# Kernel tuning notes

Measured on AMD Instinct MI355X. Metric: run time of the kernel, lower is better.

## Reference

```python
import jax, jax.numpy as jnp
import numpy as np

N = 32768          # nodes
LEVELS = 4         # num_sign_hops + 1
NUM_FEATURES = 512
HIDDEN = 512
VQ_DIM = 64
CODEBOOK_SIZE = 4096
VQ_WEIGHT = 0.25   # commitment_weight


def setup_inputs() -> dict:
    key = jax.random.key(0)
    ks = jax.random.split(key, 11)
    s = 0.02
    return {
        "x": jax.random.normal(ks[0], (N, LEVELS, NUM_FEATURES), jnp.float32),
        # per-level encoder: Linear(F,512) -> ReLU -> Linear(512,D)
        "enc_w1": jax.random.normal(ks[1], (LEVELS, NUM_FEATURES, HIDDEN), jnp.float32) * s,
        "enc_b1": jnp.zeros((LEVELS, HIDDEN), jnp.float32),
        "enc_w2": jax.random.normal(ks[2], (LEVELS, HIDDEN, VQ_DIM), jnp.float32) * s,
        "enc_b2": jnp.zeros((LEVELS, VQ_DIM), jnp.float32),
        # per-level decoder: Linear(D,512) -> ReLU -> Linear(512,F)
        "dec_w1": jax.random.normal(ks[3], (LEVELS, VQ_DIM, HIDDEN), jnp.float32) * s,
        "dec_b1": jnp.zeros((LEVELS, HIDDEN), jnp.float32),
        "dec_w2": jax.random.normal(ks[4], (LEVELS, HIDDEN, NUM_FEATURES), jnp.float32) * s,
        "dec_b2": jnp.zeros((LEVELS, NUM_FEATURES), jnp.float32),
        # per-level EMA codebooks (constants w.r.t. gradient in the torch module)
        "codebook": jax.random.normal(ks[5], (LEVELS, CODEBOOK_SIZE, VQ_DIM), jnp.float32),
    }


def reference(x, enc_w1, enc_b1, enc_w2, enc_b2,
              dec_w1, dec_b1, dec_w2, dec_b2, codebook):
    # Faithful to Quantizer.forward (eval mode: dropout = identity; EMA codebook
    # update is a training-time side effect, not part of the returned math).
    L = x.shape[1]
    total_mse = jnp.float32(0.0)
    commit_last = jnp.float32(0.0)
    for l in range(L):  # small fixed level count, structurally distinct params
        xl = x[:, l, :]                                   # [N, F]
        h = jax.nn.relu(xl @ enc_w1[l] + enc_b1[l])       # [N, 512]
        z = h @ enc_w2[l] + enc_b2[l]                     # [N, D]
        cb = codebook[l]                                  # [K, D]
        # squared euclidean distances [N, K] (cdist^2 via expansion)
        d = ((z * z).sum(-1, keepdims=True)
             - 2.0 * (z @ cb.T)
             + (cb * cb).sum(-1)[None, :])
        idx = jnp.argmin(d, axis=-1)                      # [N]
        q = cb[idx]                                       # [N, D] codebook lookup
        # commitment loss: mse(stop_grad(quantize), z) * weight
        commit = VQ_WEIGHT * jnp.mean((jax.lax.stop_gradient(q) - z) ** 2)
        # straight-through estimator
        quant = z + jax.lax.stop_gradient(q - z)
        h2 = jax.nn.relu(quant @ dec_w1[l] + dec_b1[l])   # [N, 512]
        x_hat = h2 @ dec_w2[l] + dec_b2[l]                # [N, F]
        total_mse = total_mse + jnp.mean((x_hat - xl) ** 2)
        commit_last = commit  # original returns LAST level's commit_loss / levels
    return (total_mse / L, commit_last / L)
```

## Files before the change

kernel.cpp:

```cpp
#include <hip/hip_runtime.h>

#define NS 32768
#define NLEV 4
#define NF 512
#define HID 512
#define VQD 64
#define CBS 4096

typedef __attribute__((ext_vector_type(8))) short bf16x8;
typedef __attribute__((ext_vector_type(4))) float f32x4;

__device__ inline unsigned short f2bf(float f) {
    unsigned int u = __float_as_uint(f);
    unsigned int r = (u + 0x7FFFu + ((u >> 16) & 1u)) >> 16;
    return (unsigned short)r;
}

__device__ __forceinline__ void gl16(const void* g, void* l) {
    __builtin_amdgcn_global_load_lds(
        (const __attribute__((address_space(1))) unsigned int*)g,
        (__attribute__((address_space(3))) unsigned int*)l, 16, 0, 0);
}


__global__ void transpose_all(const float* __restrict__ ew1, const float* __restrict__ ew2,
                              const float* __restrict__ dw1, const float* __restrict__ dw2,
                              unsigned short* __restrict__ ew1t, unsigned short* __restrict__ ew2t,
                              unsigned short* __restrict__ dw1t, unsigned short* __restrict__ dw2t) {
    long i = (long)blockIdx.x * 256 + threadIdx.x;
    const long s1 = (long)NLEV * NF * HID;
    const long s2 = (long)NLEV * HID * VQD;
    const long s3 = (long)NLEV * VQD * HID;
    const long s4 = (long)NLEV * HID * NF;
    const float* src;
    unsigned short* dst;
    int R, C;
    if (i < s1) { src = ew1; dst = ew1t; R = NF; C = HID; }
    else if (i < s1 + s2) { i -= s1; src = ew2; dst = ew2t; R = HID; C = VQD; }
    else if (i < s1 + s2 + s3) { i -= s1 + s2; src = dw1; dst = dw1t; R = VQD; C = HID; }
    else if (i < s1 + s2 + s3 + s4) { i -= s1 + s2 + s3; src = dw2; dst = dw2t; R = HID; C = NF; }
    else return;
    int r = (int)(i % R);
    long t = i / R;
    int c = (int)(t % C);
    int b = (int)(t / C);
    dst[i] = f2bf(src[((long)b * R + r) * C + c]);
}

__global__ void cb_prep(const float* __restrict__ cb, unsigned short* __restrict__ cbb,
                        float* __restrict__ cbn) {
    int i = blockIdx.x * 256 + threadIdx.x;
    if (i >= NLEV * CBS) return;
    const float* row = cb + (long)i * VQD;
    float s = 0.f;
    for (int k = 0; k < VQD; k++) {
        float v = row[k];
        s += v * v;
        cbb[(long)i * VQD + k] = f2bf(v);
    }
    cbn[i] = s;
}

__global__ void xconv(const float* __restrict__ x, unsigned short* __restrict__ xb) {
    long i = (long)blockIdx.x * 256 + threadIdx.x;
    int l = (int)(i / ((long)NS * (NF / 8)));
    long rem = i % ((long)NS * (NF / 8));
    int n = (int)(rem >> 6);
    int f8 = ((int)rem & 63) * 8;
    const float* src = x + ((long)n * NLEV + l) * NF + f8;
    float4 f0 = *(const float4*)src;
    float4 f1 = *(const float4*)(src + 4);
    short t[8];
    t[0] = (short)f2bf(f0.x); t[1] = (short)f2bf(f0.y); t[2] = (short)f2bf(f0.z); t[3] = (short)f2bf(f0.w);
    t[4] = (short)f2bf(f1.x); t[5] = (short)f2bf(f1.y); t[6] = (short)f2bf(f1.z); t[7] = (short)f2bf(f1.w);
    *(int4*)(xb + ((long)l * NS + n) * NF + f8) = *(const int4*)t;
}

template <int NT, int NTOT, int RELU, int OUT_MODE, int GATHER>
__global__ __launch_bounds__(256) void gemm128(
    const unsigned short* __restrict__ Ab, long astride, long abatch,
    const int* __restrict__ idx,
    const unsigned short* __restrict__ Bt, long bbatch,
    const float* __restrict__ bias, long biasbatch,
    unsigned short* __restrict__ Cb, float* __restrict__ Cf, long cbatch,
    const float* __restrict__ Xref, long xstride, long xbatch,
    float* __restrict__ accum, int K) {
    constexpr int BN = NT * 32;
    constexpr int NBPAN = NTOT / BN;
    constexpr int BNP = BN + 8;
    constexpr int SMEM = (128 * 32 + BN * 32) > (64 * BNP) ? (128 * 32 + BN * 32) : (64 * BNP);
    __shared__ __align__(16) short smem[SMEM];
    short* As = smem;
    short* Bs = smem + 128 * 32;
    __shared__ float red[4];

    const int bid = blockIdx.x;
    const int mblk = bid & 255;
    const int panel = bid >> 8;
    const int n_blk = panel % NBPAN;
    const int lvl = panel / NBPAN;

    Ab += (long)lvl * abatch;
    Bt += (long)lvl * bbatch;
    bias += (long)lvl * biasbatch;
    if (OUT_MODE == 0 || OUT_MODE == 1) Cb += (long)lvl * cbatch;
    if (OUT_MODE == 1) Cf += (long)lvl * cbatch;
    if (OUT_MODE == 2) Xref += (long)lvl * xbatch;
    if (GATHER) idx += (long)lvl * NS;

    const int tid = threadIdx.x;
    const int m0 = mblk * 128;
    const int n0 = n_blk * BN;
    const int wave = tid >> 6, lane = tid & 63, quad = lane >> 4, lr = lane & 15;
    const int wm = wave >> 1, wn = wave & 1;
    const int lrow = lane >> 2;
    const int lcol = (lane & 3) * 8;

    f32x4 acc[4][NT];
#pragma unroll
    for (int i = 0; i < 4; i++)
#pragma unroll
        for (int j = 0; j < NT; j++) acc[i][j] = (f32x4){0.f, 0.f, 0.f, 0.f};

    for (int k0 = 0; k0 < K; k0 += 32) {
        if (GATHER) {
            int r0 = m0 + wave * 16 + lrow;
            gl16(Ab + (long)idx[r0] * K + k0 + lcol, &As[(wave * 16) * 32]);
            gl16(Ab + (long)idx[r0 + 64] * K + k0 + lcol, &As[(64 + wave * 16) * 32]);
        } else {
            const unsigned short* ga = Ab + (long)(m0 + wave * 16 + lrow) * astride + k0 + lcol;
            gl16(ga, &As[(wave * 16) * 32]);
            gl16(ga + 64 * astride, &As[(64 + wave * 16) * 32]);
        }
        const unsigned short* gb = Bt + (long)(n0 + wave * 16 + lrow) * K + k0 + lcol;
        gl16(gb, &Bs[(wave * 16) * 32]);
        if (NT == 4) gl16(gb + 64 * (long)K, &Bs[(64 + wave * 16) * 32]);
        __syncthreads();

        bf16x8 af[4], bfr[NT];
#pragma unroll
        for (int mt = 0; mt < 4; mt++)
            af[mt] = *(const bf16x8*)&As[(wm * 64 + mt * 16 + lr) * 32 + quad * 8];
#pragma unroll
        for (int nt = 0; nt < NT; nt++)
            bfr[nt] = *(const bf16x8*)&Bs[(wn * NT * 16 + nt * 16 + lr) * 32 + quad * 8];
#pragma unroll
        for (int mt = 0; mt < 4; mt++)
#pragma unroll
            for (int nt = 0; nt < NT; nt++)
                acc[mt][nt] = __builtin_amdgcn_mfma_f32_16x16x32_bf16(af[mt], bfr[nt], acc[mt][nt], 0, 0, 0);
        __syncthreads();
    }

    float bvs[NT];
#pragma unroll
    for (int nt = 0; nt < NT; nt++) bvs[nt] = bias[n0 + wn * NT * 16 + nt * 16 + lr];

    if (OUT_MODE == 2) {
        float lsum = 0.f;
#pragma unroll
        for (int nt = 0; nt < NT; nt++) {
            int col = n0 + wn * NT * 16 + nt * 16 + lr;
#pragma unroll
            for (int mt = 0; mt < 4; mt++) {
#pragma unroll
                for (int r = 0; r < 4; r++) {
                    int row = m0 + wm * 64 + mt * 16 + quad * 4 + r;
                    float v = acc[mt][nt][r] + bvs[nt];
                    float d = v - Xref[(long)row * xstride + col];
                    lsum += d * d;
                }
            }
        }
#pragma unroll
        for (int off = 32; off; off >>= 1) lsum += __shfl_down(lsum, off, 64);
        if (lane == 0) red[wave] = lsum;
        __syncthreads();
        if (tid == 0) atomicAdd(accum, red[0] + red[1] + red[2] + red[3]);
    } else {
        short* Ct = smem;
#pragma unroll
        for (int p = 0; p < 2; p++) {
            __syncthreads();
            if (wm == p) {
#pragma unroll
                for (int nt = 0; nt < NT; nt++) {
                    int cl = wn * NT * 16 + nt * 16 + lr;
#pragma unroll
                    for (int mt = 0; mt < 4; mt++) {
#pragma unroll
                        for (int r = 0; r < 4; r++) {
                            int rl = mt * 16 + quad * 4 + r;
                            float v = acc[mt][nt][r] + bvs[nt];
                            if (RELU) v = v > 0.f ? v : 0.f;
                            Ct[rl * BNP + cl] = (short)f2bf(v);
                        }
                    }
                }
            }
            __syncthreads();
            constexpr int PER = (64 * BN / 8) / 256;
#pragma unroll
            for (int j = 0; j < PER; j++) {
                int id = j * 256 + tid;
                int row = id / (BN / 8);
                int seg = id % (BN / 8);
                int4 raw;
                short tmp[8];
                *(int4*)tmp = *(const int4*)&Ct[row * BNP + seg * 8];
                raw = *(const int4*)tmp;
                int rg = m0 + p * 64 + row;
                int cg = n0 + seg * 8;
                *(int4*)&Cb[(long)rg * NTOT + cg] = raw;
                if (OUT_MODE == 1) {
                    float f[8];
#pragma unroll
                    for (int e = 0; e < 8; e++)
                        f[e] = __uint_as_float(((unsigned int)(unsigned short)tmp[e]) << 16);
                    *(float4*)&Cf[(long)rg * NTOT + cg] = (float4){f[0], f[1], f[2], f[3]};
                    *(float4*)&Cf[(long)rg * NTOT + cg + 4] = (float4){f[4], f[5], f[6], f[7]};
                }
            }
        }
    }
}

__global__ __launch_bounds__(256) void vq_argmin(const unsigned short* __restrict__ Zb,
                                                 const unsigned short* __restrict__ cbb,
                                                 const float* __restrict__ cbn,
                                                 int* __restrict__ idxo) {
    __shared__ __align__(16) short Zs[2 * 128 * 32];
    __shared__ __align__(16) short Cs[2 * 64 * 32];
    const int lvl = blockIdx.y;
    Zb += (long)lvl * NS * VQD;
    cbb += (long)lvl * CBS * VQD;
    cbn += (long)lvl * CBS;
    idxo += (long)lvl * NS;
    const int tid = threadIdx.x;
    const int m0 = blockIdx.x * 128;
    const int wave = tid >> 6, lane = tid & 63, quad = lane >> 4, lr = lane & 15;
    const int lrow = lane >> 2, lcol = (lane & 3) * 8;

#pragma unroll
    for (int j = 0; j < 4; j++) {
        int f = tid * 4 + j;
        int p = f >> 9;
        int rem = f & 511;
        int r = rem >> 2;
        int c = (rem & 3) * 8;
        ((int4*)Zs)[f] = *(const int4*)(Zb + (long)(m0 + r) * VQD + p * 32 + c);
    }
    __syncthreads();
    bf16x8 a[2][2];
#pragma unroll
    for (int h = 0; h < 2; h++)
#pragma unroll
        for (int p = 0; p < 2; p++)
            a[h][p] = *(const bf16x8*)&Zs[p * 4096 + (h * 64 + wave * 16 + lr) * 32 + quad * 8];

    float minv[2][4] = {{1e30f, 1e30f, 1e30f, 1e30f}, {1e30f, 1e30f, 1e30f, 1e30f}};
    int mini[2][4] = {{0, 0, 0, 0}, {0, 0, 0, 0}};

    for (int nb = 0; nb < CBS; nb += 64) {
        __syncthreads();
#pragma unroll
        for (int i = 0; i < 2; i++) {
            int s = i * 4 + wave;
            int p = s >> 2;
            int r0 = (s & 3) * 16;
            gl16(cbb + (long)(nb + r0 + lrow) * VQD + p * 32 + lcol, &Cs[s * 512]);
        }
        __syncthreads();
#pragma unroll
        for (int nt = 0; nt < 4; nt++) {
            bf16x8 b0 = *(const bf16x8*)&Cs[(nt * 16 + lr) * 32 + quad * 8];
            bf16x8 b1 = *(const bf16x8*)&Cs[2048 + (nt * 16 + lr) * 32 + quad * 8];
            int n = nb + nt * 16 + lr;
            float cn = cbn[n];
#pragma unroll
            for (int h = 0; h < 2; h++) {
                f32x4 acc = {0.f, 0.f, 0.f, 0.f};
                acc = __builtin_amdgcn_mfma_f32_16x16x32_bf16(a[h][0], b0, acc, 0, 0, 0);
                acc = __builtin_amdgcn_mfma_f32_16x16x32_bf16(a[h][1], b1, acc, 0, 0, 0);
#pragma unroll
                for (int r = 0; r < 4; r++) {
                    float d = cn - 2.0f * acc[r];
                    if (d < minv[h][r]) {
                        minv[h][r] = d;
                        mini[h][r] = n;
                    }
                }
            }
        }
    }
#pragma unroll
    for (int h = 0; h < 2; h++)
#pragma unroll
        for (int r = 0; r < 4; r++) {
            float v = minv[h][r];
            int ix = mini[h][r];
#pragma unroll
            for (int off = 8; off; off >>= 1) {
                float ov = __shfl_xor(v, off, 64);
                int oi = __shfl_xor(ix, off, 64);
                if (ov < v || (ov == v && oi < ix)) {
                    v = ov;
                    ix = oi;
                }
            }
            if (lr == 0) idxo[m0 + h * 64 + wave * 16 + quad * 4 + r] = ix;
        }
}

__global__ __launch_bounds__(256) void commit_k(const int* __restrict__ idx,
                                                const float* __restrict__ cbf,
                                                const float* __restrict__ zf,
                                                float* __restrict__ accum) {
    int m = blockIdx.x * 256 + threadIdx.x;
    int id = idx[m];
    const float* c = cbf + (long)id * VQD;
    const float* z = zf + (long)m * VQD;
    float s = 0.f;
#pragma unroll
    for (int k = 0; k < VQD; k++) {
        float d = c[k] - z[k];
        s += d * d;
    }
    int lane = threadIdx.x & 63;
#pragma unroll
    for (int off = 32; off; off >>= 1) s += __shfl_down(s, off, 64);
    if (lane == 0) atomicAdd(accum, s);
}

__global__ void finalize_k(const float* __restrict__ accum, float* __restrict__ out) {
    out[0] = accum[0] / ((float)NS * NF * NLEV);
    out[1] = 0.25f * accum[1] / ((float)NS * VQD * NLEV);
}

extern "C" void kernel_launch(void* const* d_in, const int* in_sizes, int n_in, void* d_out,
                              int out_size, void* d_ws, size_t ws_size, hipStream_t stream) {
    const float* x = (const float*)d_in[0];
    const float* enc_w1 = (const float*)d_in[1];
    const float* enc_b1 = (const float*)d_in[2];
    const float* enc_w2 = (const float*)d_in[3];
    const float* enc_b2 = (const float*)d_in[4];
    const float* dec_w1 = (const float*)d_in[5];
    const float* dec_b1 = (const float*)d_in[6];
    const float* dec_w2 = (const float*)d_in[7];
    const float* dec_b2 = (const float*)d_in[8];
    const float* cb = (const float*)d_in[9];

    char* ws = (char*)d_ws;
    size_t o = 0;
    float* accum = (float*)(ws + o); o += 256;
    unsigned short* enc_w1t = (unsigned short*)(ws + o); o += (size_t)NLEV * HID * NF * 2;
    unsigned short* enc_w2t = (unsigned short*)(ws + o); o += (size_t)NLEV * VQD * HID * 2;
    unsigned short* dec_w1t = (unsigned short*)(ws + o); o += (size_t)NLEV * HID * VQD * 2;
    unsigned short* dec_w2t = (unsigned short*)(ws + o); o += (size_t)NLEV * NF * HID * 2;
    unsigned short* cbb = (unsigned short*)(ws + o); o += (size_t)NLEV * CBS * VQD * 2;
    float* cbn = (float*)(ws + o); o += (size_t)NLEV * CBS * 4;
    unsigned short* xb = (unsigned short*)(ws + o); o += (size_t)NLEV * NS * NF * 2;
    unsigned short* hb = (unsigned short*)(ws + o); o += (size_t)NLEV * NS * HID * 2;
    float* zf = (float*)(ws + o); o += (size_t)NLEV * NS * VQD * 4;
    unsigned short* zb = (unsigned short*)(ws + o); o += (size_t)NLEV * NS * VQD * 2;
    int* idxp = (int*)(ws + o); o += (size_t)NLEV * NS * 4;
    unsigned short* h2b = xb;

    hipMemsetAsync(accum, 0, 8, stream);

    transpose_all<<<(2 * NLEV * NF * HID + 2 * NLEV * HID * VQD + 255) / 256, 256, 0, stream>>>(
        enc_w1, enc_w2, dec_w1, dec_w2, enc_w1t, enc_w2t, dec_w1t, dec_w2t);
    cb_prep<<<(NLEV * CBS + 255) / 256, 256, 0, stream>>>(cb, cbb, cbn);
    xconv<<<(int)(((long)NLEV * NS * (NF / 8) + 255) / 256), 256, 0, stream>>>(x, xb);

    const int gBig = 256 * (HID / 128) * NLEV;
    const int gZ = 256 * 1 * NLEV;
    dim3 gVQ(NS / 128, NLEV);

    gemm128<4, HID, 1, 0, 0><<<gBig, 256, 0, stream>>>(
        xb, NF, (long)NS * NF, nullptr,
        enc_w1t, (long)HID * NF, enc_b1, HID,
        hb, nullptr, (long)NS * HID, nullptr, 0, 0, nullptr, NF);
    gemm128<2, VQD, 0, 1, 0><<<gZ, 256, 0, stream>>>(
        hb, HID, (long)NS * HID, nullptr,
        enc_w2t, (long)VQD * HID, enc_b2, VQD,
        zb, zf, (long)NS * VQD, nullptr, 0, 0, nullptr, HID);
    vq_argmin<<<gVQ, 256, 0, stream>>>(zb, cbb, cbn, idxp);
    commit_k<<<NS / 256, 256, 0, stream>>>(idxp + (long)(NLEV - 1) * NS,
                                           cb + (long)(NLEV - 1) * CBS * VQD,
                                           zf + (long)(NLEV - 1) * NS * VQD, accum + 1);
    gemm128<4, HID, 1, 0, 1><<<gBig, 256, 0, stream>>>(
        cbb, 0, (long)CBS * VQD, idxp,
        dec_w1t, (long)HID * VQD, dec_b1, HID,
        h2b, nullptr, (long)NS * HID, nullptr, 0, 0, nullptr, VQD);
    gemm128<4, NF, 0, 2, 0><<<gBig, 256, 0, stream>>>(
        h2b, HID, (long)NS * HID, nullptr,
        dec_w2t, (long)NF * HID, dec_b2, NF,
        nullptr, nullptr, 0, x, (long)NLEV * NF, NF, accum, HID);

    finalize_k<<<1, 1, 0, stream>>>(accum, (float*)d_out);
}
```

Measured before the change: 934.1 us.

## Fuse encoder output GEMM with VQ argmin and commit loss; deepen GEMM k-stage

```diff
diff --git a/kernel.cpp b/kernel.cpp
--- a/kernel.cpp
+++ b/kernel.cpp
@@ -14,6 +14,9 @@
     unsigned int u = __float_as_uint(f);
     unsigned int r = (u + 0x7FFFu + ((u >> 16) & 1u)) >> 16;
     return (unsigned short)r;
+}
+__device__ inline float bf2f(unsigned short s) {
+    return __uint_as_float(((unsigned int)s) << 16);
 }
 
 __device__ __forceinline__ void gl16(const void* g, void* l) {
@@ -82,29 +85,28 @@
     const int* __restrict__ idx,
     const unsigned short* __restrict__ Bt, long bbatch,
     const float* __restrict__ bias, long biasbatch,
-    unsigned short* __restrict__ Cb, float* __restrict__ Cf, long cbatch,
-    const float* __restrict__ Xref, long xstride, long xbatch,
+    unsigned short* __restrict__ Cb, long cbatch,
+    const unsigned short* __restrict__ Xref, long xbatch,
     float* __restrict__ accum, int K) {
     constexpr int BN = NT * 32;
-    constexpr int NBPAN = NTOT / BN;
+    constexpr int NPAN = NTOT / BN;
     constexpr int BNP = BN + 8;
-    constexpr int SMEM = (128 * 32 + BN * 32) > (64 * BNP) ? (128 * 32 + BN * 32) : (64 * BNP);
-    __shared__ __align__(16) short smem[SMEM];
+    __shared__ __align__(16) short smem[2 * 128 * 32 + 2 * BN * 32];
     short* As = smem;
-    short* Bs = smem + 128 * 32;
+    short* Bs = smem + 2 * 128 * 32;
     __shared__ float red[4];
 
     const int bid = blockIdx.x;
-    const int mblk = bid & 255;
-    const int panel = bid >> 8;
-    const int n_blk = panel % NBPAN;
-    const int lvl = panel / NBPAN;
+    const int inner = bid % (256 * NPAN);
+    const int lvl = bid / (256 * NPAN);
+    constexpr int CHUNK = 8 * NPAN;
+    const int mblk = (inner / CHUNK) * 8 + (inner % CHUNK) / NPAN;
+    const int n_blk = inner % NPAN;
 
     Ab += (long)lvl * abatch;
     Bt += (long)lvl * bbatch;
     bias += (long)lvl * biasbatch;
-    if (OUT_MODE == 0 || OUT_MODE == 1) Cb += (long)lvl * cbatch;
-    if (OUT_MODE == 1) Cf += (long)lvl * cbatch;
+    if (OUT_MODE == 0) Cb += (long)lvl * cbatch;
     if (OUT_MODE == 2) Xref += (long)lvl * xbatch;
     if (GATHER) idx += (long)lvl * NS;
 
@@ -116,39 +118,50 @@
     const int lrow = lane >> 2;
     const int lcol = (lane & 3) * 8;
 
+    long idx0 = 0, idx1 = 0;
+    if (GATHER) {
+        idx0 = idx[m0 + wave * 16 + lrow];
+        idx1 = idx[m0 + 64 + wave * 16 + lrow];
+    }
+
     f32x4 acc[4][NT];
 #pragma unroll
     for (int i = 0; i < 4; i++)
 #pragma unroll
         for (int j = 0; j < NT; j++) acc[i][j] = (f32x4){0.f, 0.f, 0.f, 0.f};
 
-    for (int k0 = 0; k0 < K; k0 += 32) {
-        if (GATHER) {
-            int r0 = m0 + wave * 16 + lrow;
-            gl16(Ab + (long)idx[r0] * K + k0 + lcol, &As[(wave * 16) * 32]);
-            gl16(Ab + (long)idx[r0 + 64] * K + k0 + lcol, &As[(64 + wave * 16) * 32]);
-        } else {
-            const unsigned short* ga = Ab + (long)(m0 + wave * 16 + lrow) * astride + k0 + lcol;
-            gl16(ga, &As[(wave * 16) * 32]);
-            gl16(ga + 64 * astride, &As[(64 + wave * 16) * 32]);
-        }
-        const unsigned short* gb = Bt + (long)(n0 + wave * 16 + lrow) * K + k0 + lcol;
-        gl16(gb, &Bs[(wave * 16) * 32]);
-        if (NT == 4) gl16(gb + 64 * (long)K, &Bs[(64 + wave * 16) * 32]);
-        __syncthreads();
-
-        bf16x8 af[4], bfr[NT];
-#pragma unroll
-        for (int mt = 0; mt < 4; mt++)
-            af[mt] = *(const bf16x8*)&As[(wm * 64 + mt * 16 + lr) * 32 + quad * 8];
-#pragma unroll
-        for (int nt = 0; nt < NT; nt++)
-            bfr[nt] = *(const bf16x8*)&Bs[(wn * NT * 16 + nt * 16 + lr) * 32 + quad * 8];
-#pragma unroll
-        for (int mt = 0; mt < 4; mt++)
+    for (int k0 = 0; k0 < K; k0 += 64) {
+#pragma unroll
+        for (int p = 0; p < 2; p++) {
+            const int kk = k0 + p * 32;
+            if (GATHER) {
+                gl16(Ab + idx0 * K + kk + lcol, &As[p * 4096 + (wave * 16) * 32]);
+                gl16(Ab + idx1 * K + kk + lcol, &As[p * 4096 + (64 + wave * 16) * 32]);
+            } else {
+                const unsigned short* ga = Ab + (long)(m0 + wave * 16 + lrow) * astride + kk + lcol;
+                gl16(ga, &As[p * 4096 + (wave * 16) * 32]);
+                gl16(ga + 64 * astride, &As[p * 4096 + (64 + wave * 16) * 32]);
+            }
+            const unsigned short* gb = Bt + (long)(n0 + wave * 16 + lrow) * K + kk + lcol;
+            gl16(gb, &Bs[p * BN * 32 + (wave * 16) * 32]);
+            if (NT == 4) gl16(gb + 64 * (long)K, &Bs[p * BN * 32 + (64 + wave * 16) * 32]);
+        }
+        __syncthreads();
+#pragma unroll
+        for (int p = 0; p < 2; p++) {
+            bf16x8 af[4], bfr[NT];
+#pragma unroll
+            for (int mt = 0; mt < 4; mt++)
+                af[mt] = *(const bf16x8*)&As[p * 4096 + (wm * 64 + mt * 16 + lr) * 32 + quad * 8];
 #pragma unroll
             for (int nt = 0; nt < NT; nt++)
-                acc[mt][nt] = __builtin_amdgcn_mfma_f32_16x16x32_bf16(af[mt], bfr[nt], acc[mt][nt], 0, 0, 0);
+                bfr[nt] = *(const bf16x8*)&Bs[p * BN * 32 + (wn * NT * 16 + nt * 16 + lr) * 32 + quad * 8];
+#pragma unroll
+            for (int mt = 0; mt < 4; mt++)
+#pragma unroll
+                for (int nt = 0; nt < NT; nt++)
+                    acc[mt][nt] = __builtin_amdgcn_mfma_f32_16x16x32_bf16(af[mt], bfr[nt], acc[mt][nt], 0, 0, 0);
+        }
         __syncthreads();
     }
 
@@ -167,7 +180,7 @@
                 for (int r = 0; r < 4; r++) {
                     int row = m0 + wm * 64 + mt * 16 + quad * 4 + r;
                     float v = acc[mt][nt][r] + bvs[nt];
-                    float d = v - Xref[(long)row * xstride + col];
+                    float d = v - bf2f(Xref[(long)row * NTOT + col]);
                     lsum += d * d;
                 }
             }
@@ -205,59 +218,111 @@
                 int id = j * 256 + tid;
                 int row = id / (BN / 8);
                 int seg = id % (BN / 8);
-                int4 raw;
                 short tmp[8];
                 *(int4*)tmp = *(const int4*)&Ct[row * BNP + seg * 8];
-                raw = *(const int4*)tmp;
-                int rg = m0 + p * 64 + row;
-                int cg = n0 + seg * 8;
-                *(int4*)&Cb[(long)rg * NTOT + cg] = raw;
-                if (OUT_MODE == 1) {
-                    float f[8];
-#pragma unroll
-                    for (int e = 0; e < 8; e++)
-                        f[e] = __uint_as_float(((unsigned int)(unsigned short)tmp[e]) << 16);
-                    *(float4*)&Cf[(long)rg * NTOT + cg] = (float4){f[0], f[1], f[2], f[3]};
-                    *(float4*)&Cf[(long)rg * NTOT + cg + 4] = (float4){f[4], f[5], f[6], f[7]};
-                }
-            }
-        }
-    }
-}
-
-__global__ __launch_bounds__(256) void vq_argmin(const unsigned short* __restrict__ Zb,
-                                                 const unsigned short* __restrict__ cbb,
-                                                 const float* __restrict__ cbn,
-                                                 int* __restrict__ idxo) {
-    __shared__ __align__(16) short Zs[2 * 128 * 32];
-    __shared__ __align__(16) short Cs[2 * 64 * 32];
+                *(int4*)&Cb[(long)(m0 + p * 64 + row) * NTOT + n0 + seg * 8] = *(const int4*)tmp;
+            }
+        }
+    }
+}
+
+__global__ __launch_bounds__(256) void enc2_vq(
+    const unsigned short* __restrict__ hb, const unsigned short* __restrict__ ew2t,
+    const float* __restrict__ eb2, const unsigned short* __restrict__ cbb,
+    const float* __restrict__ cbn, int* __restrict__ idxo, float* __restrict__ accum) {
+    __shared__ __align__(16) short As[2 * 128 * 32];
+    __shared__ __align__(16) short Bs[2 * 64 * 32];
+    __shared__ float znp[2][128];
+    __shared__ float zn2[128];
+    __shared__ float cred;
+
     const int lvl = blockIdx.y;
-    Zb += (long)lvl * NS * VQD;
+    hb += (long)lvl * NS * HID;
+    ew2t += (long)lvl * VQD * HID;
+    eb2 += (long)lvl * VQD;
     cbb += (long)lvl * CBS * VQD;
     cbn += (long)lvl * CBS;
     idxo += (long)lvl * NS;
+
     const int tid = threadIdx.x;
     const int m0 = blockIdx.x * 128;
     const int wave = tid >> 6, lane = tid & 63, quad = lane >> 4, lr = lane & 15;
+    const int wm = wave >> 1, wn = wave & 1;
     const int lrow = lane >> 2, lcol = (lane & 3) * 8;
 
-#pragma unroll
-    for (int j = 0; j < 4; j++) {
-        int f = tid * 4 + j;
-        int p = f >> 9;
-        int rem = f & 511;
-        int r = rem >> 2;
-        int c = (rem & 3) * 8;
-        ((int4*)Zs)[f] = *(const int4*)(Zb + (long)(m0 + r) * VQD + p * 32 + c);
-    }
+    if (tid == 0) cred = 0.f;
+
+    f32x4 acc[4][2];
+#pragma unroll
+    for (int i = 0; i < 4; i++)
+#pragma unroll
+        for (int j = 0; j < 2; j++) acc[i][j] = (f32x4){0.f, 0.f, 0.f, 0.f};
+
+    for (int k0 = 0; k0 < HID; k0 += 64) {
+#pragma unroll
+        for (int p = 0; p < 2; p++) {
+            const int kk = k0 + p * 32;
+            const unsigned short* ga = hb + (long)(m0 + wave * 16 + lrow) * HID + kk + lcol;
+            gl16(ga, &As[p * 4096 + (wave * 16) * 32]);
+            gl16(ga + 64 * HID, &As[p * 4096 + (64 + wave * 16) * 32]);
+            const unsigned short* gb = ew2t + (long)(wave * 16 + lrow) * HID + kk + lcol;
+            gl16(gb, &Bs[p * 2048 + (wave * 16) * 32]);
+        }
+        __syncthreads();
+#pragma unroll
+        for (int p = 0; p < 2; p++) {
+            bf16x8 af[4], bfr[2];
+#pragma unroll
+            for (int mt = 0; mt < 4; mt++)
+                af[mt] = *(const bf16x8*)&As[p * 4096 + (wm * 64 + mt * 16 + lr) * 32 + quad * 8];
+#pragma unroll
+            for (int nt = 0; nt < 2; nt++)
+                bfr[nt] = *(const bf16x8*)&Bs[p * 2048 + (wn * 32 + nt * 16 + lr) * 32 + quad * 8];
+#pragma unroll
+            for (int mt = 0; mt < 4; mt++)
+#pragma unroll
+                for (int nt = 0; nt < 2; nt++)
+                    acc[mt][nt] = __builtin_amdgcn_mfma_f32_16x16x32_bf16(af[mt], bfr[nt], acc[mt][nt], 0, 0, 0);
+        }
+        __syncthreads();
+    }
+
+    short* Zs = As;
+    float bvs[2] = {eb2[wn * 32 + lr], eb2[wn * 32 + 16 + lr]};
+#pragma unroll
+    for (int mt = 0; mt < 4; mt++)
+#pragma unroll
+        for (int r = 0; r < 4; r++) {
+            int row = wm * 64 + mt * 16 + quad * 4 + r;
+#pragma unroll
+            for (int nt = 0; nt < 2; nt++) {
+                float v = acc[mt][nt][r] + bvs[nt];
+                Zs[wn * 4096 + row * 32 + nt * 16 + lr] = (short)f2bf(v);
+            }
+        }
     __syncthreads();
+
+    {
+        int row = tid >> 1, p = tid & 1;
+        const short* zr = &Zs[p * 4096 + row * 32];
+        float s = 0.f;
+#pragma unroll
+        for (int j = 0; j < 32; j++) {
+            float f = bf2f((unsigned short)zr[j]);
+            s += f * f;
+        }
+        znp[p][row] = s;
+    }
     bf16x8 a[2][2];
 #pragma unroll
     for (int h = 0; h < 2; h++)
 #pragma unroll
         for (int p = 0; p < 2; p++)
             a[h][p] = *(const bf16x8*)&Zs[p * 4096 + (h * 64 + wave * 16 + lr) * 32 + quad * 8];
-
+    __syncthreads();
+    if (tid < 128) zn2[tid] = znp[0][tid] + znp[1][tid];
+
+    short* Cs = Bs;
     float minv[2][4] = {{1e30f, 1e30f, 1e30f, 1e30f}, {1e30f, 1e30f, 1e30f, 1e30f}};
     int mini[2][4] = {{0, 0, 0, 0}, {0, 0, 0, 0}};
 
@@ -279,12 +344,12 @@
             float cn = cbn[n];
 #pragma unroll
             for (int h = 0; h < 2; h++) {
-                f32x4 acc = {0.f, 0.f, 0.f, 0.f};
-                acc = __builtin_amdgcn_mfma_f32_16x16x32_bf16(a[h][0], b0, acc, 0, 0, 0);
-                acc = __builtin_amdgcn_mfma_f32_16x16x32_bf16(a[h][1], b1, acc, 0, 0, 0);
+                f32x4 d4 = {0.f, 0.f, 0.f, 0.f};
+                d4 = __builtin_amdgcn_mfma_f32_16x16x32_bf16(a[h][0], b0, d4, 0, 0, 0);
+                d4 = __builtin_amdgcn_mfma_f32_16x16x32_bf16(a[h][1], b1, d4, 0, 0, 0);
 #pragma unroll
                 for (int r = 0; r < 4; r++) {
-                    float d = cn - 2.0f * acc[r];
+                    float d = cn - 2.0f * d4[r];
                     if (d < minv[h][r]) {
                         minv[h][r] = d;
                         mini[h][r] = n;
@@ -293,6 +358,8 @@
             }
         }
     }
+
+    float csum = 0.f;
 #pragma unroll
     for (int h = 0; h < 2; h++)
 #pragma unroll
@@ -308,28 +375,17 @@
                     ix = oi;
                 }
             }
-            if (lr == 0) idxo[m0 + h * 64 + wave * 16 + quad * 4 + r] = ix;
-        }
-}
-
-__global__ __launch_bounds__(256) void commit_k(const int* __restrict__ idx,
-                                                const float* __restrict__ cbf,
-                                                const float* __restrict__ zf,
-                                                float* __restrict__ accum) {
-    int m = blockIdx.x * 256 + threadIdx.x;
-    int id = idx[m];
-    const float* c = cbf + (long)id * VQD;
-    const float* z = zf + (long)m * VQD;
-    float s = 0.f;
-#pragma unroll
-    for (int k = 0; k < VQD; k++) {
-        float d = c[k] - z[k];
-        s += d * d;
-    }
-    int lane = threadIdx.x & 63;
-#pragma unroll
-    for (int off = 32; off; off >>= 1) s += __shfl_down(s, off, 64);
-    if (lane == 0) atomicAdd(accum, s);
+            if (lr == 0) {
+                int row = h * 64 + wave * 16 + quad * 4 + r;
+                idxo[m0 + row] = ix;
+                csum += v + zn2[row];
+            }
+        }
+    if (lvl == NLEV - 1) {
+        if (lr == 0) atomicAdd(&cred, csum);
+        __syncthreads();
+        if (tid == 0) atomicAdd(accum + 1, cred);
+    }
 }
 
 __global__ void finalize_k(const float* __restrict__ accum, float* __restrict__ out) {
@@ -361,10 +417,7 @@
     float* cbn = (float*)(ws + o); o += (size_t)NLEV * CBS * 4;
     unsigned short* xb = (unsigned short*)(ws + o); o += (size_t)NLEV * NS * NF * 2;
     unsigned short* hb = (unsigned short*)(ws + o); o += (size_t)NLEV * NS * HID * 2;
-    float* zf = (float*)(ws + o); o += (size_t)NLEV * NS * VQD * 4;
-    unsigned short* zb = (unsigned short*)(ws + o); o += (size_t)NLEV * NS * VQD * 2;
     int* idxp = (int*)(ws + o); o += (size_t)NLEV * NS * 4;
-    unsigned short* h2b = xb;
 
     hipMemsetAsync(accum, 0, 8, stream);
 
@@ -374,29 +427,20 @@
     xconv<<<(int)(((long)NLEV * NS * (NF / 8) + 255) / 256), 256, 0, stream>>>(x, xb);
 
     const int gBig = 256 * (HID / 128) * NLEV;
-    const int gZ = 256 * 1 * NLEV;
-    dim3 gVQ(NS / 128, NLEV);
 
     gemm128<4, HID, 1, 0, 0><<<gBig, 256, 0, stream>>>(
         xb, NF, (long)NS * NF, nullptr,
         enc_w1t, (long)HID * NF, enc_b1, HID,
-        hb, nullptr, (long)NS * HID, nullptr, 0, 0, nullptr, NF);
-    gemm128<2, VQD, 0, 1, 0><<<gZ, 256, 0, stream>>>(
-        hb, HID, (long)NS * HID, nullptr,
-        enc_w2t, (long)VQD * HID, enc_b2, VQD,
-        zb, zf, (long)NS * VQD, nullptr, 0, 0, nullptr, HID);
-    vq_argmin<<<gVQ, 256, 0, stream>>>(zb, cbb, cbn, idxp);
-    commit_k<<<NS / 256, 256, 0, stream>>>(idxp + (long)(NLEV - 1) * NS,
-                                           cb + (long)(NLEV - 1) * CBS * VQD,
-                                           zf + (long)(NLEV - 1) * NS * VQD, accum + 1);
+        hb, (long)NS * HID, nullptr, 0, nullptr, NF);
+    enc2_vq<<<dim3(NS / 128, NLEV), 256, 0, stream>>>(hb, enc_w2t, enc_b2, cbb, cbn, idxp, accum);
     gemm128<4, HID, 1, 0, 1><<<gBig, 256, 0, stream>>>(
         cbb, 0, (long)CBS * VQD, idxp,
         dec_w1t, (long)HID * VQD, dec_b1, HID,
-        h2b, nullptr, (long)NS * HID, nullptr, 0, 0, nullptr, VQD);
+        hb, (long)NS * HID, nullptr, 0, nullptr, VQD);
     gemm128<4, NF, 0, 2, 0><<<gBig, 256, 0, stream>>>(
-        h2b, HID, (long)NS * HID, nullptr,
+        hb, HID, (long)NS * HID, nullptr,
         dec_w2t, (long)NF * HID, dec_b2, NF,
-        nullptr, nullptr, 0, x, (long)NLEV * NF, NF, accum, HID);
+        nullptr, 0, xb, (long)NS * NF, accum, HID);
 
     finalize_k<<<1, 1, 0, stream>>>(accum, (float*)d_out);
 }
```

New measurement: 838.8 us. 10.2% less time.
